# Optimization experiments

Measured on AMD Instinct MI355X. Metric: run time of the kernel, lower is better.

The kernel has to match this reference:

```python
import jax, jax.numpy as jnp
import numpy as np

C = 64
CQK = C // 8  # query/key channels = 8


def setup_inputs() -> dict:
    key = jax.random.key(0)
    ks = jax.random.split(key, 7)
    B, D, H, W = 1, 16, 32, 32
    x = jax.random.normal(ks[0], (B, C, D, H, W), dtype=jnp.float32)
    # 1x1x1 Conv3d weights collapse to [out_ch, in_ch] matrices; std=0.01 per nn.init.normal_
    wq = 0.01 * jax.random.normal(ks[1], (CQK, C), dtype=jnp.float32)
    bq = jnp.zeros((CQK,), dtype=jnp.float32)
    wk = 0.01 * jax.random.normal(ks[2], (CQK, C), dtype=jnp.float32)
    bk = jnp.zeros((CQK,), dtype=jnp.float32)
    wv = 0.01 * jax.random.normal(ks[3], (C, C), dtype=jnp.float32)
    bv = jnp.zeros((C,), dtype=jnp.float32)
    gamma = jnp.zeros((1,), dtype=jnp.float32)  # nn.Parameter(torch.zeros(1))
    return {"x": x, "wq": wq, "bq": bq, "wk": wk, "bk": bk, "wv": wv, "bv": bv, "gamma": gamma}


def reference(x, wq, bq, wk, bk, wv, bv, gamma):
    B, Cc, D, H, W = x.shape
    N = D * H * W
    xf = x.reshape(B, Cc, N)  # [B, C, N]
    # 1x1x1 convs == per-position linear projections
    q = jnp.einsum('oc,bcn->bon', wq, xf) + bq[None, :, None]   # [B, CQK, N]
    k = jnp.einsum('oc,bcn->bon', wk, xf) + bk[None, :, None]   # [B, CQK, N]
    v = jnp.einsum('oc,bcn->bon', wv, xf) + bv[None, :, None]   # [B, C, N]
    # attention[b, i, j] = softmax_j( q[:, :, i] . k[:, :, j] )  -> [B, N, N]
    scores = jnp.einsum('bon,bom->bnm', q, k)
    attn = jax.nn.softmax(scores, axis=-1)
    # out[b, c, i] = sum_j v[b, c, j] * attn[b, i, j]
    out = jnp.einsum('bcm,bnm->bcn', v, attn).reshape(B, Cc, D, H, W)
    return x + gamma * out
```

## Files before the change

### kernel.cpp

```cpp
#include <hip/hip_runtime.h>

#define NPOS 16384
#define KSPLIT 8
#define KEYS_PER_BLK (NPOS / KSPLIT)
#define CHUNK 512
#define LOG2E 1.4426950408889634f

typedef short bf16x8 __attribute__((ext_vector_type(8)));
typedef unsigned short u16x8 __attribute__((ext_vector_type(8)));
typedef float floatx16 __attribute__((ext_vector_type(16)));
typedef float floatx2 __attribute__((ext_vector_type(2)));

static __device__ __forceinline__ unsigned short f2bf(float f) {
    return (unsigned short)(__builtin_bit_cast(unsigned int, f) >> 16);
}
static __device__ __forceinline__ float bf2f(unsigned short h) {
    return __builtin_bit_cast(float, (unsigned int)h << 16);
}

#if __has_builtin(__builtin_amdgcn_exp2f)
static __device__ __forceinline__ float exp2_fast(float x) {
    return __builtin_amdgcn_exp2f(x);
}
#else
static __device__ __forceinline__ float exp2_fast(float x) {
    float r;
    asm("v_exp_f32 %0, %1" : "=v"(r) : "v"(x));
    return r;
}
#endif

static __device__ __forceinline__ unsigned int pk_bf16(float e_even, float e_odd) {
    return __builtin_amdgcn_perm(__builtin_bit_cast(unsigned int, e_odd),
                                 __builtin_bit_cast(unsigned int, e_even),
                                 0x07060302u);
}

static __device__ __forceinline__ int sigma(int n) {
    const int w12 = n & 12;
    return (w12 == 4 || w12 == 8) ? (n ^ 12) : n;
}

__global__ __launch_bounds__(256) void proj_kernel(
    const float* __restrict__ x,
    const float* __restrict__ wq, const float* __restrict__ bq,
    const float* __restrict__ wk, const float* __restrict__ bk,
    const float* __restrict__ wv, const float* __restrict__ bv,
    unsigned short* __restrict__ qb16, unsigned short* __restrict__ kb16,
    unsigned short* __restrict__ vbg16)
{
    const int t = threadIdx.x;
    const int n = blockIdx.x * 256 + t;
    const int g = blockIdx.y;

    const float* w;
    const float* b;
    if (g == 0)      { w = wq; b = bq; }
    else if (g == 1) { w = wk; b = bk; }
    else             { w = wv + (g - 2) * 8 * 64; b = bv + (g - 2) * 8; }

    float acc[8];
#pragma unroll
    for (int oo = 0; oo < 8; ++oo) acc[oo] = b[oo];
#pragma unroll 16
    for (int c = 0; c < 64; ++c) {
        const float xv = x[c * NPOS + n];
#pragma unroll
        for (int oo = 0; oo < 8; ++oo)
            acc[oo] = fmaf(w[oo * 64 + c], xv, acc[oo]);
    }

    if (g == 0) {
        u16x8 qp;
#pragma unroll
        for (int j = 0; j < 8; ++j) qp[j] = f2bf(acc[j] * LOG2E);
        ((uint4*)qb16)[n] = __builtin_bit_cast(uint4, qp);
    } else if (g == 1) {
        u16x8 kp;
#pragma unroll
        for (int j = 0; j < 8; ++j) kp[j] = f2bf(acc[j]);
        ((uint4*)kb16)[n] = __builtin_bit_cast(uint4, kp);
    } else {
        const int o0 = (g - 2) * 8;
        const int np = sigma(n);
        const size_t base = (size_t)(np >> 3) * 512 + (np & 7);
#pragma unroll
        for (int oo = 0; oo < 8; ++oo)
            vbg16[base + (size_t)(o0 + oo) * 8] = f2bf(acc[oo]);
    }
}

__global__ __launch_bounds__(256, 4) void attn_kernel(
    const uint4* __restrict__ qb4,
    const uint4* __restrict__ kb4,
    const uint4* __restrict__ vbg4,
    unsigned short* __restrict__ nump,
    float* __restrict__ denp)
{
    __shared__ __align__(16) char smem[8448];
    uint4* k_lds = (uint4*)smem;

    const int t     = threadIdx.x;
    const int wave  = t >> 6;
    const int lane  = t & 63;
    const int m     = lane & 31;
    const int half  = lane >> 5;
    const int qhalf = wave >> 1;
    const int khalf = wave & 1;

    const int qblk = blockIdx.x >> 3;
    const int kq   = blockIdx.x & 7;
    const int i0   = qblk * 64;
    const int jb   = kq * KEYS_PER_BLK;

    uint4 qa4 = (half == 0) ? qb4[i0 + qhalf * 32 + m] : make_uint4(0, 0, 0, 0);
    const bf16x8 bqf = __builtin_bit_cast(bf16x8, qa4);

    floatx16 accA = {};
    floatx16 accB = {};
    floatx2  dacc[2];
    dacc[0] = (floatx2){0.f, 0.f};
    dacc[1] = (floatx2){0.f, 0.f};

#pragma unroll 1
    for (int c4 = 0; c4 < 4; ++c4) {
        const int j0 = jb + c4 * CHUNK;
        __syncthreads();
        k_lds[t]       = kb4[j0 + t];
        k_lds[256 + t] = kb4[j0 + 256 + t];
        __syncthreads();

        const int kwb = khalf * 256;
#pragma unroll 2
        for (int st = 0; st < 8; ++st) {
            const int kb_ = kwb + st * 32;
            const bf16x8 ak = __builtin_bit_cast(bf16x8, k_lds[kb_ + m]);
            const floatx16 s = __builtin_amdgcn_mfma_f32_32x32x16_bf16(
                ak, bqf, (floatx16){}, 0, 0, 0);

            float e[16];
#pragma unroll
            for (int r = 0; r < 16; ++r) e[r] = exp2_fast(s[r]);
#pragma unroll
            for (int p = 0; p < 8; ++p)
                dacc[p & 1] += (floatx2){e[2 * p], e[2 * p + 1]};
            unsigned int P[8];
#pragma unroll
            for (int p = 0; p < 8; ++p) P[p] = pk_bf16(e[2 * p], e[2 * p + 1]);

            const int g8t = (j0 + kb_) >> 3;
#pragma unroll
            for (int f = 0; f < 2; ++f) {
                uint4 afu;
                afu.x = P[4 * f + 0];
                afu.y = P[4 * f + 1];
                afu.z = P[4 * f + 2];
                afu.w = P[4 * f + 3];
                const bf16x8 af = __builtin_bit_cast(bf16x8, afu);

                const int g8 = g8t + f * 2 + half;
                const bf16x8 v0 = __builtin_bit_cast(
                    bf16x8, vbg4[(size_t)g8 * 64 + m]);
                const bf16x8 v1 = __builtin_bit_cast(
                    bf16x8, vbg4[(size_t)g8 * 64 + 32 + m]);
                accA = __builtin_amdgcn_mfma_f32_32x32x16_bf16(af, v0, accA,
                                                               0, 0, 0);
                accB = __builtin_amdgcn_mfma_f32_32x32x16_bf16(af, v1, accB,
                                                               0, 0, 0);
            }
        }
    }

    const floatx2 dfold = dacc[0] + dacc[1];
    const float dl = dfold[0] + dfold[1];
    const float dw = dl + __shfl_xor(dl, 32);

    __syncthreads();
    float*          xden = (float*)smem;
    unsigned short* xacc = (unsigned short*)(smem + 256);
    const int recl = qhalf * 64 + lane;
    if (khalf == 1) {
        if (half == 0) xden[qhalf * 32 + m] = dw;
        u16x8 a0, a1, a2, a3;
#pragma unroll
        for (int j = 0; j < 8; ++j) {
            a0[j] = f2bf(accA[j]);
            a1[j] = f2bf(accA[8 + j]);
            a2[j] = f2bf(accB[j]);
            a3[j] = f2bf(accB[8 + j]);
        }
        uint4* dst = (uint4*)(xacc + recl * 32);
        dst[0] = __builtin_bit_cast(uint4, a0);
        dst[1] = __builtin_bit_cast(uint4, a1);
        dst[2] = __builtin_bit_cast(uint4, a2);
        dst[3] = __builtin_bit_cast(uint4, a3);
    }
    __syncthreads();
    if (khalf == 0) {
        const uint4* src = (const uint4*)(xacc + recl * 32);
        const u16x8 b0 = __builtin_bit_cast(u16x8, src[0]);
        const u16x8 b1 = __builtin_bit_cast(u16x8, src[1]);
        const u16x8 b2 = __builtin_bit_cast(u16x8, src[2]);
        const u16x8 b3 = __builtin_bit_cast(u16x8, src[3]);
        u16x8 o0, o1, o2, o3;
#pragma unroll
        for (int j = 0; j < 8; ++j) {
            o0[j] = f2bf(accA[j]      + bf2f(b0[j]));
            o1[j] = f2bf(accA[8 + j]  + bf2f(b1[j]));
            o2[j] = f2bf(accB[j]      + bf2f(b2[j]));
            o3[j] = f2bf(accB[8 + j]  + bf2f(b3[j]));
        }
        const size_t base =
            ((((size_t)kq * 256 + qblk) * 2 + qhalf) * 64 + lane) * 32;
        uint4* gdst = (uint4*)(nump + base);
        gdst[0] = __builtin_bit_cast(uint4, o0);
        gdst[1] = __builtin_bit_cast(uint4, o1);
        gdst[2] = __builtin_bit_cast(uint4, o2);
        gdst[3] = __builtin_bit_cast(uint4, o3);
        if (half == 0)
            denp[(size_t)kq * NPOS + i0 + qhalf * 32 + m] =
                dw + xden[qhalf * 32 + m];
    }
}

__global__ __launch_bounds__(256) void finalize_kernel(
    const float* __restrict__ x,
    const unsigned short* __restrict__ nump,
    const float* __restrict__ denp,
    const float* __restrict__ gamma,
    float* __restrict__ out)
{
    const int b    = blockIdx.x;
    const int qblk = b >> 1;
    const int qh   = b & 1;
    const int t    = threadIdx.x;
    const int lane = t >> 2;
    const int u    = t & 3;
    const int n0   = qblk * 64 + qh * 32;

    __shared__ float dsum[32];
    __shared__ float ot[32 * 66];
    if (t < 32) dsum[t] = 0.f;
    __syncthreads();
    atomicAdd(&dsum[t & 31], denp[(size_t)(t >> 5) * NPOS + n0 + (t & 31)]);

    float ns[8];
#pragma unroll
    for (int j = 0; j < 8; ++j) ns[j] = 0.f;
#pragma unroll
    for (int kq = 0; kq < 8; ++kq) {
        const size_t base =
            ((((size_t)kq * 256 + qblk) * 2 + qh) * 64 + lane) * 32 + u * 8;
        const u16x8 h = __builtin_bit_cast(u16x8, *(const uint4*)(nump + base));
#pragma unroll
        for (int j = 0; j < 8; ++j) ns[j] += bf2f(h[j]);
    }

    const int clow = lane & 31;
    const int hf   = lane >> 5;
#pragma unroll
    for (int j = 0; j < 8; ++j) {
        const int off = u * 8 + j;
        const int r   = off & 15;
        const int row = (r & 3) + 8 * (r >> 2) + 4 * hf;
        const int c   = (off >> 4) * 32 + clow;
        ot[row * 66 + c] = ns[j];
    }
    __syncthreads();

    const float g  = gamma[0];
    const int   c2 = t >> 2;
    const int   nq = t & 3;
    const int   nb = nq * 8;
#pragma unroll
    for (int j = 0; j < 8; ++j) {
        const int row = nb + j;
        const size_t gi = (size_t)c2 * NPOS + n0 + row;
        out[gi] = fmaf(g, ot[row * 66 + c2] *
                              __builtin_amdgcn_rcpf(dsum[row]), x[gi]);
    }
}

extern "C" void kernel_launch(void* const* d_in, const int* in_sizes, int n_in,
                              void* d_out, int out_size, void* d_ws, size_t ws_size,
                              hipStream_t stream)
{
    (void)in_sizes; (void)n_in; (void)out_size; (void)ws_size;

    const float* x     = (const float*)d_in[0];
    const float* wq    = (const float*)d_in[1];
    const float* bq    = (const float*)d_in[2];
    const float* wk    = (const float*)d_in[3];
    const float* bk    = (const float*)d_in[4];
    const float* wv    = (const float*)d_in[5];
    const float* bv    = (const float*)d_in[6];
    const float* gamma = (const float*)d_in[7];
    float* out = (float*)d_out;

    char* ws = (char*)d_ws;
    unsigned short* qb16  = (unsigned short*)(ws);
    unsigned short* kb16  = (unsigned short*)(ws + 262144);
    unsigned short* vbg16 = (unsigned short*)(ws + 524288);
    unsigned short* nump  = (unsigned short*)(ws + 2621440);
    float*          denp  = (float*)(ws + 19398656);

    proj_kernel<<<dim3(NPOS / 256, 10), 256, 0, stream>>>(
        x, wq, bq, wk, bk, wv, bv, qb16, kb16, vbg16);
    attn_kernel<<<(NPOS / 64) * KSPLIT, 256, 0, stream>>>(
        (const uint4*)qb16, (const uint4*)kb16, (const uint4*)vbg16,
        nump, denp);
    finalize_kernel<<<512, 256, 0, stream>>>(x, nump, denp, gamma, out);
}
```

Baseline: 138.0 us.

## Process two query tiles per wave to reuse K and V fragments

Each wave now computes two 32-query tiles against every key tile, so one K fragment from LDS and the V fragments from global memory feed twice the MFMA work. The block covers 128 queries, which halves the attention grid, and the partial-numerator layout is re-indexed by 32-query tile. The cost is doubled accumulator registers, a larger LDS reduction buffer, and fewer blocks (1024 instead of 2048), which may lower occupancy or latency hiding. The inner loop unroll also drops from 2 to 1.

```diff
diff --git a/kernel.cpp b/kernel.cpp
--- a/kernel.cpp
+++ b/kernel.cpp
@@ -97,7 +97,7 @@
     unsigned short* __restrict__ nump,
     float* __restrict__ denp)
 {
-    __shared__ __align__(16) char smem[8448];
+    __shared__ __align__(16) char smem[16896];
     uint4* k_lds = (uint4*)smem;
 
     const int t     = threadIdx.x;
@@ -105,22 +105,24 @@
     const int lane  = t & 63;
     const int m     = lane & 31;
     const int half  = lane >> 5;
-    const int qhalf = wave >> 1;
+    const int qpair = wave >> 1;
     const int khalf = wave & 1;
 
     const int qblk = blockIdx.x >> 3;
     const int kq   = blockIdx.x & 7;
-    const int i0   = qblk * 64;
+    const int i0   = qblk * 128;
     const int jb   = kq * KEYS_PER_BLK;
-
-    uint4 qa4 = (half == 0) ? qb4[i0 + qhalf * 32 + m] : make_uint4(0, 0, 0, 0);
-    const bf16x8 bqf = __builtin_bit_cast(bf16x8, qa4);
-
-    floatx16 accA = {};
-    floatx16 accB = {};
-    floatx2  dacc[2];
-    dacc[0] = (floatx2){0.f, 0.f};
-    dacc[1] = (floatx2){0.f, 0.f};
+    const int qt0  = (i0 >> 5) + qpair * 2;
+
+    const uint4 zero4 = make_uint4(0, 0, 0, 0);
+    const uint4 qLo4 = (half == 0) ? qb4[i0 + qpair * 64 + m]      : zero4;
+    const uint4 qHi4 = (half == 0) ? qb4[i0 + qpair * 64 + 32 + m] : zero4;
+    const bf16x8 bqLo = __builtin_bit_cast(bf16x8, qLo4);
+    const bf16x8 bqHi = __builtin_bit_cast(bf16x8, qHi4);
+
+    floatx16 accLoA = {}, accLoB = {};
+    floatx16 accHiA = {}, accHiB = {};
+    floatx2  dLo = {0.f, 0.f}, dHi = {0.f, 0.f};
 
 #pragma unroll 1
     for (int c4 = 0; c4 < 4; ++c4) {
@@ -131,95 +133,144 @@
         __syncthreads();
 
         const int kwb = khalf * 256;
-#pragma unroll 2
+#pragma unroll 1
         for (int st = 0; st < 8; ++st) {
             const int kb_ = kwb + st * 32;
             const bf16x8 ak = __builtin_bit_cast(bf16x8, k_lds[kb_ + m]);
-            const floatx16 s = __builtin_amdgcn_mfma_f32_32x32x16_bf16(
-                ak, bqf, (floatx16){}, 0, 0, 0);
-
-            float e[16];
-#pragma unroll
-            for (int r = 0; r < 16; ++r) e[r] = exp2_fast(s[r]);
-#pragma unroll
-            for (int p = 0; p < 8; ++p)
-                dacc[p & 1] += (floatx2){e[2 * p], e[2 * p + 1]};
-            unsigned int P[8];
-#pragma unroll
-            for (int p = 0; p < 8; ++p) P[p] = pk_bf16(e[2 * p], e[2 * p + 1]);
+            const floatx16 sLo = __builtin_amdgcn_mfma_f32_32x32x16_bf16(
+                ak, bqLo, (floatx16){}, 0, 0, 0);
+            const floatx16 sHi = __builtin_amdgcn_mfma_f32_32x32x16_bf16(
+                ak, bqHi, (floatx16){}, 0, 0, 0);
 
             const int g8t = (j0 + kb_) >> 3;
+            bf16x8 vf0[2], vf1[2];
 #pragma unroll
             for (int f = 0; f < 2; ++f) {
-                uint4 afu;
-                afu.x = P[4 * f + 0];
-                afu.y = P[4 * f + 1];
-                afu.z = P[4 * f + 2];
-                afu.w = P[4 * f + 3];
-                const bf16x8 af = __builtin_bit_cast(bf16x8, afu);
-
                 const int g8 = g8t + f * 2 + half;
-                const bf16x8 v0 = __builtin_bit_cast(
-                    bf16x8, vbg4[(size_t)g8 * 64 + m]);
-                const bf16x8 v1 = __builtin_bit_cast(
-                    bf16x8, vbg4[(size_t)g8 * 64 + 32 + m]);
-                accA = __builtin_amdgcn_mfma_f32_32x32x16_bf16(af, v0, accA,
-                                                               0, 0, 0);
-                accB = __builtin_amdgcn_mfma_f32_32x32x16_bf16(af, v1, accB,
-                                                               0, 0, 0);
-            }
-        }
-    }
-
-    const floatx2 dfold = dacc[0] + dacc[1];
-    const float dl = dfold[0] + dfold[1];
-    const float dw = dl + __shfl_xor(dl, 32);
+                vf0[f] = __builtin_bit_cast(bf16x8, vbg4[(size_t)g8 * 64 + m]);
+                vf1[f] = __builtin_bit_cast(bf16x8,
+                                            vbg4[(size_t)g8 * 64 + 32 + m]);
+            }
+
+            {
+                float e[16];
+#pragma unroll
+                for (int r = 0; r < 16; ++r) e[r] = exp2_fast(sLo[r]);
+#pragma unroll
+                for (int p = 0; p < 8; ++p)
+                    dLo += (floatx2){e[2 * p], e[2 * p + 1]};
+                unsigned int P[8];
+#pragma unroll
+                for (int p = 0; p < 8; ++p)
+                    P[p] = pk_bf16(e[2 * p], e[2 * p + 1]);
+#pragma unroll
+                for (int f = 0; f < 2; ++f) {
+                    uint4 afu;
+                    afu.x = P[4 * f + 0];
+                    afu.y = P[4 * f + 1];
+                    afu.z = P[4 * f + 2];
+                    afu.w = P[4 * f + 3];
+                    const bf16x8 af = __builtin_bit_cast(bf16x8, afu);
+                    accLoA = __builtin_amdgcn_mfma_f32_32x32x16_bf16(
+                        af, vf0[f], accLoA, 0, 0, 0);
+                    accLoB = __builtin_amdgcn_mfma_f32_32x32x16_bf16(
+                        af, vf1[f], accLoB, 0, 0, 0);
+                }
+            }
+            {
+                float e[16];
+#pragma unroll
+                for (int r = 0; r < 16; ++r) e[r] = exp2_fast(sHi[r]);
+#pragma unroll
+                for (int p = 0; p < 8; ++p)
+                    dHi += (floatx2){e[2 * p], e[2 * p + 1]};
+                unsigned int P[8];
+#pragma unroll
+                for (int p = 0; p < 8; ++p)
+                    P[p] = pk_bf16(e[2 * p], e[2 * p + 1]);
+#pragma unroll
+                for (int f = 0; f < 2; ++f) {
+                    uint4 afu;
+                    afu.x = P[4 * f + 0];
+                    afu.y = P[4 * f + 1];
+                    afu.z = P[4 * f + 2];
+                    afu.w = P[4 * f + 3];
+                    const bf16x8 af = __builtin_bit_cast(bf16x8, afu);
+                    accHiA = __builtin_amdgcn_mfma_f32_32x32x16_bf16(
+                        af, vf0[f], accHiA, 0, 0, 0);
+                    accHiB = __builtin_amdgcn_mfma_f32_32x32x16_bf16(
+                        af, vf1[f], accHiB, 0, 0, 0);
+                }
+            }
+        }
+    }
+
+    const float dlLo = dLo[0] + dLo[1];
+    const float dwLo = dlLo + __shfl_xor(dlLo, 32);
+    const float dlHi = dHi[0] + dHi[1];
+    const float dwHi = dlHi + __shfl_xor(dlHi, 32);
 
     __syncthreads();
     float*          xden = (float*)smem;
-    unsigned short* xacc = (unsigned short*)(smem + 256);
-    const int recl = qhalf * 64 + lane;
+    unsigned short* xacc = (unsigned short*)(smem + 512);
     if (khalf == 1) {
-        if (half == 0) xden[qhalf * 32 + m] = dw;
-        u16x8 a0, a1, a2, a3;
-#pragma unroll
-        for (int j = 0; j < 8; ++j) {
-            a0[j] = f2bf(accA[j]);
-            a1[j] = f2bf(accA[8 + j]);
-            a2[j] = f2bf(accB[j]);
-            a3[j] = f2bf(accB[8 + j]);
-        }
-        uint4* dst = (uint4*)(xacc + recl * 32);
-        dst[0] = __builtin_bit_cast(uint4, a0);
-        dst[1] = __builtin_bit_cast(uint4, a1);
-        dst[2] = __builtin_bit_cast(uint4, a2);
-        dst[3] = __builtin_bit_cast(uint4, a3);
+        if (half == 0) {
+            xden[(qpair * 2 + 0) * 32 + m] = dwLo;
+            xden[(qpair * 2 + 1) * 32 + m] = dwHi;
+        }
+#pragma unroll
+        for (int tile = 0; tile < 2; ++tile) {
+            const floatx16* aA = tile ? &accHiA : &accLoA;
+            const floatx16* aB = tile ? &accHiB : &accLoB;
+            u16x8 a0, a1, a2, a3;
+#pragma unroll
+            for (int j = 0; j < 8; ++j) {
+                a0[j] = f2bf((*aA)[j]);
+                a1[j] = f2bf((*aA)[8 + j]);
+                a2[j] = f2bf((*aB)[j]);
+                a3[j] = f2bf((*aB)[8 + j]);
+            }
+            uint4* dst = (uint4*)(xacc + ((qpair * 2 + tile) * 64 + lane) * 32);
+            dst[0] = __builtin_bit_cast(uint4, a0);
+            dst[1] = __builtin_bit_cast(uint4, a1);
+            dst[2] = __builtin_bit_cast(uint4, a2);
+            dst[3] = __builtin_bit_cast(uint4, a3);
+        }
     }
     __syncthreads();
     if (khalf == 0) {
-        const uint4* src = (const uint4*)(xacc + recl * 32);
-        const u16x8 b0 = __builtin_bit_cast(u16x8, src[0]);
-        const u16x8 b1 = __builtin_bit_cast(u16x8, src[1]);
-        const u16x8 b2 = __builtin_bit_cast(u16x8, src[2]);
-        const u16x8 b3 = __builtin_bit_cast(u16x8, src[3]);
-        u16x8 o0, o1, o2, o3;
-#pragma unroll
-        for (int j = 0; j < 8; ++j) {
-            o0[j] = f2bf(accA[j]      + bf2f(b0[j]));
-            o1[j] = f2bf(accA[8 + j]  + bf2f(b1[j]));
-            o2[j] = f2bf(accB[j]      + bf2f(b2[j]));
-            o3[j] = f2bf(accB[8 + j]  + bf2f(b3[j]));
-        }
-        const size_t base =
-            ((((size_t)kq * 256 + qblk) * 2 + qhalf) * 64 + lane) * 32;
-        uint4* gdst = (uint4*)(nump + base);
-        gdst[0] = __builtin_bit_cast(uint4, o0);
-        gdst[1] = __builtin_bit_cast(uint4, o1);
-        gdst[2] = __builtin_bit_cast(uint4, o2);
-        gdst[3] = __builtin_bit_cast(uint4, o3);
-        if (half == 0)
-            denp[(size_t)kq * NPOS + i0 + qhalf * 32 + m] =
-                dw + xden[qhalf * 32 + m];
+#pragma unroll
+        for (int tile = 0; tile < 2; ++tile) {
+            const floatx16* aA = tile ? &accHiA : &accLoA;
+            const floatx16* aB = tile ? &accHiB : &accLoB;
+            const uint4* src =
+                (const uint4*)(xacc + ((qpair * 2 + tile) * 64 + lane) * 32);
+            const u16x8 b0 = __builtin_bit_cast(u16x8, src[0]);
+            const u16x8 b1 = __builtin_bit_cast(u16x8, src[1]);
+            const u16x8 b2 = __builtin_bit_cast(u16x8, src[2]);
+            const u16x8 b3 = __builtin_bit_cast(u16x8, src[3]);
+            u16x8 o0, o1, o2, o3;
+#pragma unroll
+            for (int j = 0; j < 8; ++j) {
+                o0[j] = f2bf((*aA)[j]      + bf2f(b0[j]));
+                o1[j] = f2bf((*aA)[8 + j]  + bf2f(b1[j]));
+                o2[j] = f2bf((*aB)[j]      + bf2f(b2[j]));
+                o3[j] = f2bf((*aB)[8 + j]  + bf2f(b3[j]));
+            }
+            const size_t base =
+                (((size_t)kq * 512 + qt0 + tile) * 64 + lane) * 32;
+            uint4* gdst = (uint4*)(nump + base);
+            gdst[0] = __builtin_bit_cast(uint4, o0);
+            gdst[1] = __builtin_bit_cast(uint4, o1);
+            gdst[2] = __builtin_bit_cast(uint4, o2);
+            gdst[3] = __builtin_bit_cast(uint4, o3);
+        }
+        if (half == 0) {
+            denp[(size_t)kq * NPOS + (qt0 + 0) * 32 + m] =
+                dwLo + xden[(qpair * 2 + 0) * 32 + m];
+            denp[(size_t)kq * NPOS + (qt0 + 1) * 32 + m] =
+                dwHi + xden[(qpair * 2 + 1) * 32 + m];
+        }
     }
 }
 
@@ -231,12 +282,10 @@
     float* __restrict__ out)
 {
     const int b    = blockIdx.x;
-    const int qblk = b >> 1;
-    const int qh   = b & 1;
     const int t    = threadIdx.x;
     const int lane = t >> 2;
     const int u    = t & 3;
-    const int n0   = qblk * 64 + qh * 32;
+    const int n0   = b * 32;
 
     __shared__ float dsum[32];
     __shared__ float ot[32 * 66];
@@ -250,7 +299,7 @@
 #pragma unroll
     for (int kq = 0; kq < 8; ++kq) {
         const size_t base =
-            ((((size_t)kq * 256 + qblk) * 2 + qh) * 64 + lane) * 32 + u * 8;
+            (((size_t)kq * 512 + b) * 64 + lane) * 32 + u * 8;
         const u16x8 h = __builtin_bit_cast(u16x8, *(const uint4*)(nump + base));
 #pragma unroll
         for (int j = 0; j < 8; ++j) ns[j] += bf2f(h[j]);
@@ -271,10 +320,9 @@
     const float g  = gamma[0];
     const int   c2 = t >> 2;
     const int   nq = t & 3;
-    const int   nb = nq * 8;
 #pragma unroll
     for (int j = 0; j < 8; ++j) {
-        const int row = nb + j;
+        const int row = nq * 8 + j;
         const size_t gi = (size_t)c2 * NPOS + n0 + row;
         out[gi] = fmaf(g, ot[row * 66 + c2] *
                               __builtin_amdgcn_rcpf(dsum[row]), x[gi]);
@@ -306,7 +354,7 @@
 
     proj_kernel<<<dim3(NPOS / 256, 10), 256, 0, stream>>>(
         x, wq, bq, wk, bk, wv, bv, qb16, kb16, vbg16);
-    attn_kernel<<<(NPOS / 64) * KSPLIT, 256, 0, stream>>>(
+    attn_kernel<<<(NPOS / 128) * KSPLIT, 256, 0, stream>>>(
         (const uint4*)qb16, (const uint4*)kb16, (const uint4*)vbg16,
         nump, denp);
     finalize_kernel<<<512, 256, 0, stream>>>(x, nump, denp, gamma, out);
```

Result: faster. 132.9 us (-3.7%).
